# Optimization experiments

Hardware: AMD Instinct MI355X
Metric: run time of the kernel (lower is better)

The kernel has to match this reference:

```python
import jax, jax.numpy as jnp
import numpy as np

N_NODES = 100000


def gcn_conv(x, src, dst, W, b, n_nodes):
    # PyG GCNConv: linear transform, add self-loops, symmetric normalization,
    # scatter-add aggregation, then bias.
    h = x @ W  # [N, out]
    # append self-loops
    loop = jnp.arange(n_nodes, dtype=src.dtype)
    s = jnp.concatenate([src, loop])
    d = jnp.concatenate([dst, loop])
    # degree of destination nodes (edge weight 1)
    deg = jax.ops.segment_sum(jnp.ones_like(d, dtype=h.dtype), d, num_segments=n_nodes)
    dinv = jnp.where(deg > 0, jax.lax.rsqrt(deg), 0.0)
    norm = dinv[s] * dinv[d]  # [E+N]
    msg = norm[:, None] * h[s]  # gather + scale
    out = jax.ops.segment_sum(msg, d, num_segments=n_nodes)  # scatter-add
    return out + b


def setup_inputs() -> dict:
    key = jax.random.key(0)
    k1, k2, k3, k4, k5 = jax.random.split(key, 5)
    x = jax.random.normal(k1, (N_NODES, 128), dtype=jnp.float32)
    edge_index = jax.random.randint(k2, (2, 1600000), 0, N_NODES, dtype=jnp.int64)
    # Glorot-style init for GCN linear weights (bias zero, as in PyG default)
    W1 = jax.random.normal(k3, (128, 128), dtype=jnp.float32) * (1.0 / np.sqrt(128))
    b1 = jnp.zeros((128,), dtype=jnp.float32)
    W2 = jax.random.normal(k4, (128, 64), dtype=jnp.float32) * (1.0 / np.sqrt(128))
    b2 = jnp.zeros((64,), dtype=jnp.float32)
    return {"x": x, "edge_index": edge_index, "W1": W1, "b1": b1, "W2": W2, "b2": b2}


def reference(x, edge_index, W1, b1, W2, b2):
    src, dst = edge_index[0], edge_index[1]
    h = gcn_conv(x, src, dst, W1, b1, N_NODES)
    h = jax.nn.relu(h)
    # dropout p=0.5 with training=False -> identity (eval mode)
    out = gcn_conv(h, src, dst, W2, b2, N_NODES)
    return out
```

## Files before the change

### kernel.cpp

```cpp
#include <hip/hip_runtime.h>
#include <hip/hip_fp16.h>
#include <math.h>

#define NN 100000
#define BS 256
#define NB 391
#define NBLK 256
#define CAP 48
#define STAGE_CAP 5120

__global__ __launch_bounds__(256) void bucketA_k(const int* __restrict__ ei,
                                                 unsigned* __restrict__ edges,
                                                 unsigned* __restrict__ seg_cnt,
                                                 int E) {
    __shared__ unsigned cur[NB];
    const int tid = threadIdx.x;
    int odd = ei[2 * (tid & 63) + 1];
    const int st = (__ballot(odd != 0) == 0ull) ? 2 : 1;
    for (int i = tid; i < NB; i += 256) cur[i] = 0;
    __syncthreads();

    const int epb = (E + NBLK - 1) / NBLK;
    const int base = blockIdx.x * epb;
    const int end = min(base + epb, E);
    unsigned* __restrict__ reg = edges + (size_t)blockIdx.x * NB * CAP;

    if (st == 2) {
        const int2* __restrict__ e2 = (const int2*)ei;
        for (int i = base + tid; i < end; i += 256) {
            unsigned s = (unsigned)e2[i].x;
            unsigned d = (unsigned)e2[(size_t)E + i].x;
            unsigned bk = d >> 8;
            unsigned pos = atomicAdd(&cur[bk], 1u);
            if (pos < CAP) reg[bk * CAP + pos] = (s << 8) | (d & 255u);
        }
    } else {
        for (int i = base + tid; i < end; i += 256) {
            unsigned s = (unsigned)ei[i];
            unsigned d = (unsigned)ei[(size_t)E + i];
            unsigned bk = d >> 8;
            unsigned pos = atomicAdd(&cur[bk], 1u);
            if (pos < CAP) reg[bk * CAP + pos] = (s << 8) | (d & 255u);
        }
    }
    __syncthreads();
    for (int i = tid; i < NB; i += 256)
        seg_cnt[(size_t)blockIdx.x * NB + i] = min(cur[i], (unsigned)CAP);
}

__global__ __launch_bounds__(512) void bucketscan_k(const unsigned* __restrict__ seg_cnt,
                                                    unsigned* __restrict__ bucket_base,
                                                    unsigned* __restrict__ row_start) {
    __shared__ unsigned tot[512];
    const int k = threadIdx.x;
    unsigned s = 0;
    if (k < NB)
        for (int b = 0; b < NBLK; ++b) s += seg_cnt[(size_t)b * NB + k];
    tot[k] = s;
    __syncthreads();
    for (int off = 1; off < 512; off <<= 1) {
        unsigned v = tot[k];
        unsigned a = (k >= off) ? tot[k - off] : 0u;
        __syncthreads();
        tot[k] = v + a;
        __syncthreads();
    }
    if (k < NB) bucket_base[k] = tot[k] - s;
    if (k == 0) row_start[NN] = tot[NB - 1];
}

__global__ __launch_bounds__(256) void bucketB_k(const unsigned* __restrict__ edges,
                                                 const unsigned* __restrict__ seg_cnt,
                                                 const unsigned* __restrict__ bucket_base,
                                                 unsigned* __restrict__ csr_src,
                                                 unsigned* __restrict__ row_start,
                                                 float* __restrict__ dinv) {
    __shared__ unsigned stage[STAGE_CAP];
    __shared__ unsigned soff[NBLK];
    __shared__ unsigned scn[256];
    __shared__ unsigned cnt[BS];
    const int k = blockIdx.x, tid = threadIdx.x;

    unsigned sc = seg_cnt[(size_t)tid * NB + k];
    scn[tid] = sc;
    __syncthreads();
    for (int off = 1; off < 256; off <<= 1) {
        unsigned v = scn[tid];
        unsigned a = (tid >= off) ? scn[tid - off] : 0u;
        __syncthreads();
        scn[tid] = v + a;
        __syncthreads();
    }
    soff[tid] = scn[tid] - sc;
    __syncthreads();
    unsigned T = scn[255];
    if (T > STAGE_CAP) T = STAGE_CAP;

    for (unsigned j = tid; j < T; j += 256) {
        int lo = 0;
        #pragma unroll
        for (int stp = 128; stp > 0; stp >>= 1) {
            int m = lo + stp;
            if (m < NBLK && soff[m] <= j) lo = m;
        }
        unsigned elem = j - soff[lo];
        stage[j] = edges[((size_t)lo * NB + k) * CAP + elem];
    }
    for (int i = tid; i < BS; i += 256) cnt[i] = 0;
    __syncthreads();

    for (unsigned j = tid; j < T; j += 256) atomicAdd(&cnt[stage[j] & 255u], 1u);
    __syncthreads();

    unsigned c0 = cnt[tid];
    scn[tid] = c0;
    __syncthreads();
    for (int off = 1; off < 256; off <<= 1) {
        unsigned v = scn[tid];
        unsigned a = (tid >= off) ? scn[tid - off] : 0u;
        __syncthreads();
        scn[tid] = v + a;
        __syncthreads();
    }
    unsigned excl = scn[tid] - c0;
    const unsigned bbase = bucket_base[k];
    unsigned g0 = (unsigned)k * BS + tid;
    if (g0 < NN) {
        row_start[g0] = bbase + excl;
        dinv[g0] = rsqrtf((float)(c0 + 1u));
    }
    __syncthreads();
    cnt[tid] = excl;
    __syncthreads();

    for (unsigned j = tid; j < T; j += 256) {
        unsigned v = stage[j];
        unsigned pos = atomicAdd(&cnt[v & 255u], 1u);
        csr_src[bbase + pos] = v >> 8;
    }
}

template <int BN, int NT>
__global__ __launch_bounds__(NT) void gemm_k128(const float* __restrict__ X,
                                                const float* __restrict__ Wm,
                                                __half* __restrict__ H) {
    constexpr int TCN = BN / 4;
    constexpr int TRN = NT / TCN;
    constexpr int TM = 8;
    constexpr int BM = TRN * TM;
    constexpr int XP = BM + 4;
    __shared__ float ws[32 * BN];
    __shared__ float xsT[128 * XP];

    const int t = threadIdx.x;
    const int tc = t % TCN;
    const int tr = t / TCN;
    const int row0 = blockIdx.x * BM;

    for (int f = t; f < BM * 32; f += NT) {
        int r = f >> 5, c4 = f & 31;
        float4 v = make_float4(0.f, 0.f, 0.f, 0.f);
        if (row0 + r < NN) v = ((const float4*)(X + (size_t)(row0 + r) * 128))[c4];
        xsT[(c4 * 4 + 0) * XP + r] = v.x;
        xsT[(c4 * 4 + 1) * XP + r] = v.y;
        xsT[(c4 * 4 + 2) * XP + r] = v.z;
        xsT[(c4 * 4 + 3) * XP + r] = v.w;
    }

    float acc[TM][4] = {};
    for (int kc = 0; kc < 4; ++kc) {
        __syncthreads();
        for (int f = t; f < 32 * BN / 4; f += NT)
            ((float4*)ws)[f] = ((const float4*)Wm)[kc * (32 * BN / 4) + f];
        __syncthreads();
        #pragma unroll 4
        for (int k2 = 0; k2 < 32; ++k2) {
            float4 bv = *(const float4*)&ws[k2 * BN + tc * 4];
            const float* __restrict__ ar = &xsT[(kc * 32 + k2) * XP + tr * TM];
            #pragma unroll
            for (int m = 0; m < TM; ++m) {
                float a = ar[m];
                acc[m][0] = fmaf(a, bv.x, acc[m][0]);
                acc[m][1] = fmaf(a, bv.y, acc[m][1]);
                acc[m][2] = fmaf(a, bv.z, acc[m][2]);
                acc[m][3] = fmaf(a, bv.w, acc[m][3]);
            }
        }
    }
    #pragma unroll
    for (int m = 0; m < TM; ++m) {
        int r = row0 + tr * TM + m;
        if (r < NN) {
            __half2 p0 = __floats2half2_rn(acc[m][0], acc[m][1]);
            __half2 p1 = __floats2half2_rn(acc[m][2], acc[m][3]);
            uint2 w;
            w.x = *(unsigned*)&p0;
            w.y = *(unsigned*)&p1;
            ((uint2*)(H + (size_t)r * BN))[tc] = w;
        }
    }
}

template <int F, bool RELU>
__global__ __launch_bounds__(256) void aggregate_k(
    const __half* __restrict__ H, const unsigned* __restrict__ row_start,
    const unsigned* __restrict__ csr_src, const float* __restrict__ dinv,
    const float* __restrict__ bias, float* __restrict__ out) {
    const int wid = (blockIdx.x * blockDim.x + threadIdx.x) >> 6;
    const int lane = threadIdx.x & 63;
    if (wid >= NN) return;

    const float di = dinv[wid];
    const unsigned s0 = row_start[wid];
    const unsigned s1 = row_start[wid + 1];

    if constexpr (F == 128) {
        const __half2* __restrict__ H2 = (const __half2*)H;
        float2 h = __half22float2(H2[(size_t)wid * 64 + lane]);
        const float w0 = di * di;
        float2 acc = make_float2(w0 * h.x, w0 * h.y);
        unsigned e = s0;
        for (; e + 4 <= s1; e += 4) {
            unsigned i0 = csr_src[e], i1 = csr_src[e + 1];
            unsigned i2 = csr_src[e + 2], i3 = csr_src[e + 3];
            float2 h0 = __half22float2(H2[(size_t)i0 * 64 + lane]);
            float2 h1v = __half22float2(H2[(size_t)i1 * 64 + lane]);
            float2 h2v = __half22float2(H2[(size_t)i2 * 64 + lane]);
            float2 h3 = __half22float2(H2[(size_t)i3 * 64 + lane]);
            float wa = di * dinv[i0], wb = di * dinv[i1];
            float wc = di * dinv[i2], wd = di * dinv[i3];
            acc.x = fmaf(wa, h0.x, acc.x);  acc.y = fmaf(wa, h0.y, acc.y);
            acc.x = fmaf(wb, h1v.x, acc.x); acc.y = fmaf(wb, h1v.y, acc.y);
            acc.x = fmaf(wc, h2v.x, acc.x); acc.y = fmaf(wc, h2v.y, acc.y);
            acc.x = fmaf(wd, h3.x, acc.x);  acc.y = fmaf(wd, h3.y, acc.y);
        }
        for (; e < s1; ++e) {
            unsigned sa = csr_src[e];
            float wa = di * dinv[sa];
            float2 ha = __half22float2(H2[(size_t)sa * 64 + lane]);
            acc.x = fmaf(wa, ha.x, acc.x);
            acc.y = fmaf(wa, ha.y, acc.y);
        }
        float2 bv = ((const float2*)bias)[lane];
        acc.x += bv.x;
        acc.y += bv.y;
        if (RELU) {
            acc.x = fmaxf(acc.x, 0.0f);
            acc.y = fmaxf(acc.y, 0.0f);
        }
        ((float2*)out)[(size_t)wid * 64 + lane] = acc;
    } else {
        float h = __half2float(H[(size_t)wid * 64 + lane]);
        float acc = di * di * h;
        unsigned e = s0;
        for (; e + 4 <= s1; e += 4) {
            unsigned i0 = csr_src[e], i1 = csr_src[e + 1];
            unsigned i2 = csr_src[e + 2], i3 = csr_src[e + 3];
            float h0 = __half2float(H[(size_t)i0 * 64 + lane]);
            float h1v = __half2float(H[(size_t)i1 * 64 + lane]);
            float h2v = __half2float(H[(size_t)i2 * 64 + lane]);
            float h3 = __half2float(H[(size_t)i3 * 64 + lane]);
            acc = fmaf(di * dinv[i0], h0, acc);
            acc = fmaf(di * dinv[i1], h1v, acc);
            acc = fmaf(di * dinv[i2], h2v, acc);
            acc = fmaf(di * dinv[i3], h3, acc);
        }
        for (; e < s1; ++e) {
            unsigned sa = csr_src[e];
            acc = fmaf(di * dinv[sa], __half2float(H[(size_t)sa * 64 + lane]), acc);
        }
        acc += bias[lane];
        if (RELU) acc = fmaxf(acc, 0.0f);
        out[(size_t)wid * 64 + lane] = acc;
    }
}

extern "C" void kernel_launch(void* const* d_in, const int* in_sizes, int n_in,
                              void* d_out, int out_size, void* d_ws, size_t ws_size,
                              hipStream_t stream) {
    const float* x  = (const float*)d_in[0];
    const int*   ei = (const int*)d_in[1];
    const float* W1 = (const float*)d_in[2];
    const float* b1 = (const float*)d_in[3];
    const float* W2 = (const float*)d_in[4];
    const float* b2 = (const float*)d_in[5];
    float* out = (float*)d_out;
    const int E = in_sizes[1] / 2;

    char* p = (char*)d_ws;
    auto take = [&](size_t n) {
        char* r = p;
        p += (n + 255) & ~(size_t)255;
        return r;
    };
    __half*   h1        = (__half*)take((size_t)NN * 128 * 2);
    float*    o1        = (float*)take((size_t)NN * 128 * 4);
    unsigned* csr_src   = (unsigned*)take((size_t)E * 4);
    unsigned* row_start = (unsigned*)take((size_t)(NN + 1) * 4);
    float*    dinvp     = (float*)take((size_t)NN * 4);
    unsigned* seg_cnt   = (unsigned*)take((size_t)NBLK * NB * 4);
    unsigned* bbase     = (unsigned*)take((size_t)NB * 4);
    unsigned* edges     = (unsigned*)h1;
    __half*   h2        = h1;

    bucketA_k<<<NBLK, 256, 0, stream>>>(ei, edges, seg_cnt, E);
    bucketscan_k<<<1, 512, 0, stream>>>(seg_cnt, bbase, row_start);
    bucketB_k<<<NB, 256, 0, stream>>>(edges, seg_cnt, bbase, csr_src, row_start, dinvp);

    const int GEMM_GRID = (NN + 63) / 64;

    gemm_k128<128, 256><<<GEMM_GRID, 256, 0, stream>>>(x, W1, h1);
    aggregate_k<128, true><<<25000, 256, 0, stream>>>(h1, row_start, csr_src, dinvp, b1, o1);

    gemm_k128<64, 128><<<GEMM_GRID, 128, 0, stream>>>(o1, W2, h2);
    aggregate_k<64, false><<<25000, 256, 0, stream>>>(h2, row_start, csr_src, dinvp, b2, out);
}
```

Measured before the change: 388.9 us.

## Use MFMA fp16 GEMMs, fp16 intermediate activations, and deeper gather unrolling

Replaces the scalar fp32 register-tiled GEMMs with MFMA 16x16x32 f16 kernels. The inputs and a pre-transposed fp16 weight copy are staged in XOR-swizzled shared memory. The first-layer aggregation now writes its output in fp16, which halves the traffic for the second GEMM's input. The aggregation loops are unrolled to 8 neighbors, with all index and feature loads issued before the FMAs to expose more memory-level parallelism. The cost is extra fp16 rounding of x and of the hidden activations, plus a small extra weight-prep kernel launch.

```diff
diff --git a/kernel.cpp b/kernel.cpp
--- a/kernel.cpp
+++ b/kernel.cpp
@@ -8,6 +8,9 @@
 #define NBLK 256
 #define CAP 48
 #define STAGE_CAP 5120
+
+typedef _Float16 half8 __attribute__((ext_vector_type(8)));
+typedef float f32x4 __attribute__((ext_vector_type(4)));
 
 __global__ __launch_bounds__(256) void bucketA_k(const int* __restrict__ ei,
                                                  unsigned* __restrict__ edges,
@@ -140,72 +143,98 @@
     }
 }
 
-template <int BN, int NT>
-__global__ __launch_bounds__(NT) void gemm_k128(const float* __restrict__ X,
-                                                const float* __restrict__ Wm,
-                                                __half* __restrict__ H) {
-    constexpr int TCN = BN / 4;
-    constexpr int TRN = NT / TCN;
-    constexpr int TM = 8;
-    constexpr int BM = TRN * TM;
-    constexpr int XP = BM + 4;
-    __shared__ float ws[32 * BN];
-    __shared__ float xsT[128 * XP];
-
+__global__ __launch_bounds__(256) void prep_w_k(const float* __restrict__ W1,
+                                                const float* __restrict__ W2,
+                                                _Float16* __restrict__ w1t,
+                                                _Float16* __restrict__ w2t) {
     const int t = threadIdx.x;
-    const int tc = t % TCN;
-    const int tr = t / TCN;
-    const int row0 = blockIdx.x * BM;
-
-    for (int f = t; f < BM * 32; f += NT) {
-        int r = f >> 5, c4 = f & 31;
-        float4 v = make_float4(0.f, 0.f, 0.f, 0.f);
-        if (row0 + r < NN) v = ((const float4*)(X + (size_t)(row0 + r) * 128))[c4];
-        xsT[(c4 * 4 + 0) * XP + r] = v.x;
-        xsT[(c4 * 4 + 1) * XP + r] = v.y;
-        xsT[(c4 * 4 + 2) * XP + r] = v.z;
-        xsT[(c4 * 4 + 3) * XP + r] = v.w;
-    }
-
-    float acc[TM][4] = {};
+    if (blockIdx.x == 0) {
+        for (int i = t; i < 128 * 128; i += 256) {
+            int k = i >> 7, n = i & 127;
+            w1t[n * 128 + k] = (_Float16)W1[i];
+        }
+    } else {
+        for (int i = t; i < 128 * 64; i += 256) {
+            int k = i >> 6, n = i & 63;
+            w2t[n * 128 + k] = (_Float16)W2[i];
+        }
+    }
+}
+
+template <int BN, bool IN_F32>
+__global__ __launch_bounds__(256) void gemm_mfma_k(const void* __restrict__ Xv,
+                                                   const _Float16* __restrict__ Wt,
+                                                   _Float16* __restrict__ H) {
+    __shared__ _Float16 xs[64 * 128];
+    __shared__ _Float16 wsm[BN * 128];
+    char* xb = (char*)xs;
+    char* wb = (char*)wsm;
+    const int t = threadIdx.x;
+    const int row0 = blockIdx.x * 64;
+
+    if constexpr (IN_F32) {
+        const float* X = (const float*)Xv;
+        for (int f = t; f < 64 * 32; f += 256) {
+            int r = f >> 5, c4 = f & 31;
+            float4 v = make_float4(0.f, 0.f, 0.f, 0.f);
+            if (row0 + r < NN) v = ((const float4*)(X + (size_t)(row0 + r) * 128))[c4];
+            _Float16 h4[4] = {(_Float16)v.x, (_Float16)v.y, (_Float16)v.z, (_Float16)v.w};
+            int byte = (r * 256 + c4 * 8) ^ ((r & 7) << 4);
+            *(uint2*)(xb + byte) = *(uint2*)h4;
+        }
+    } else {
+        const _Float16* X = (const _Float16*)Xv;
+        for (int f = t; f < 64 * 16; f += 256) {
+            int r = f >> 4, c8 = f & 15;
+            uint4 v = make_uint4(0u, 0u, 0u, 0u);
+            if (row0 + r < NN) v = ((const uint4*)(X + (size_t)(row0 + r) * 128))[c8];
+            int byte = (r * 256 + c8 * 16) ^ ((r & 7) << 4);
+            *(uint4*)(xb + byte) = v;
+        }
+    }
+    for (int f = t; f < BN * 16; f += 256) {
+        int n = f >> 4, c8 = f & 15;
+        uint4 v = ((const uint4*)(Wt + (size_t)n * 128))[c8];
+        int byte = (n * 256 + c8 * 16) ^ ((n & 7) << 4);
+        *(uint4*)(wb + byte) = v;
+    }
+    __syncthreads();
+
+    const int w = t >> 6, l = t & 63;
+    const int lr = l & 15, lk = l >> 4;
+
+    f32x4 acc[BN / 16];
+    #pragma unroll
+    for (int n = 0; n < BN / 16; ++n) acc[n] = (f32x4){0.f, 0.f, 0.f, 0.f};
+
+    #pragma unroll
     for (int kc = 0; kc < 4; ++kc) {
-        __syncthreads();
-        for (int f = t; f < 32 * BN / 4; f += NT)
-            ((float4*)ws)[f] = ((const float4*)Wm)[kc * (32 * BN / 4) + f];
-        __syncthreads();
-        #pragma unroll 4
-        for (int k2 = 0; k2 < 32; ++k2) {
-            float4 bv = *(const float4*)&ws[k2 * BN + tc * 4];
-            const float* __restrict__ ar = &xsT[(kc * 32 + k2) * XP + tr * TM];
-            #pragma unroll
-            for (int m = 0; m < TM; ++m) {
-                float a = ar[m];
-                acc[m][0] = fmaf(a, bv.x, acc[m][0]);
-                acc[m][1] = fmaf(a, bv.y, acc[m][1]);
-                acc[m][2] = fmaf(a, bv.z, acc[m][2]);
-                acc[m][3] = fmaf(a, bv.w, acc[m][3]);
-            }
-        }
-    }
+        const int kbyte = kc * 64 + lk * 16;
+        const int ar = w * 16 + lr;
+        half8 a = *(const half8*)(xb + ((ar * 256 + kbyte) ^ ((ar & 7) << 4)));
+        #pragma unroll
+        for (int n = 0; n < BN / 16; ++n) {
+            const int bc = n * 16 + lr;
+            half8 b = *(const half8*)(wb + ((bc * 256 + kbyte) ^ ((bc & 7) << 4)));
+            acc[n] = __builtin_amdgcn_mfma_f32_16x16x32_f16(a, b, acc[n], 0, 0, 0);
+        }
+    }
+
     #pragma unroll
-    for (int m = 0; m < TM; ++m) {
-        int r = row0 + tr * TM + m;
-        if (r < NN) {
-            __half2 p0 = __floats2half2_rn(acc[m][0], acc[m][1]);
-            __half2 p1 = __floats2half2_rn(acc[m][2], acc[m][3]);
-            uint2 w;
-            w.x = *(unsigned*)&p0;
-            w.y = *(unsigned*)&p1;
-            ((uint2*)(H + (size_t)r * BN))[tc] = w;
-        }
-    }
-}
-
-template <int F, bool RELU>
+    for (int n = 0; n < BN / 16; ++n) {
+        #pragma unroll
+        for (int r = 0; r < 4; ++r) {
+            int rr = row0 + w * 16 + lk * 4 + r;
+            if (rr < NN) H[(size_t)rr * BN + n * 16 + lr] = (_Float16)acc[n][r];
+        }
+    }
+}
+
+template <int F, bool RELU, bool OUT_HALF>
 __global__ __launch_bounds__(256) void aggregate_k(
-    const __half* __restrict__ H, const unsigned* __restrict__ row_start,
+    const _Float16* __restrict__ H, const unsigned* __restrict__ row_start,
     const unsigned* __restrict__ csr_src, const float* __restrict__ dinv,
-    const float* __restrict__ bias, float* __restrict__ out) {
+    const float* __restrict__ bias, void* __restrict__ outv) {
     const int wid = (blockIdx.x * blockDim.x + threadIdx.x) >> 6;
     const int lane = threadIdx.x & 63;
     if (wid >= NN) return;
@@ -215,29 +244,35 @@
     const unsigned s1 = row_start[wid + 1];
 
     if constexpr (F == 128) {
-        const __half2* __restrict__ H2 = (const __half2*)H;
-        float2 h = __half22float2(H2[(size_t)wid * 64 + lane]);
+        const unsigned* __restrict__ H2 = (const unsigned*)H;
+        auto up = [](unsigned u) {
+            __half2 h = *(__half2*)&u;
+            return __half22float2(h);
+        };
+        float2 h = up(H2[(size_t)wid * 64 + lane]);
         const float w0 = di * di;
         float2 acc = make_float2(w0 * h.x, w0 * h.y);
         unsigned e = s0;
-        for (; e + 4 <= s1; e += 4) {
-            unsigned i0 = csr_src[e], i1 = csr_src[e + 1];
-            unsigned i2 = csr_src[e + 2], i3 = csr_src[e + 3];
-            float2 h0 = __half22float2(H2[(size_t)i0 * 64 + lane]);
-            float2 h1v = __half22float2(H2[(size_t)i1 * 64 + lane]);
-            float2 h2v = __half22float2(H2[(size_t)i2 * 64 + lane]);
-            float2 h3 = __half22float2(H2[(size_t)i3 * 64 + lane]);
-            float wa = di * dinv[i0], wb = di * dinv[i1];
-            float wc = di * dinv[i2], wd = di * dinv[i3];
-            acc.x = fmaf(wa, h0.x, acc.x);  acc.y = fmaf(wa, h0.y, acc.y);
-            acc.x = fmaf(wb, h1v.x, acc.x); acc.y = fmaf(wb, h1v.y, acc.y);
-            acc.x = fmaf(wc, h2v.x, acc.x); acc.y = fmaf(wc, h2v.y, acc.y);
-            acc.x = fmaf(wd, h3.x, acc.x);  acc.y = fmaf(wd, h3.y, acc.y);
+        for (; e + 8 <= s1; e += 8) {
+            unsigned idx[8], hv[8];
+            float wq[8];
+            #pragma unroll
+            for (int q = 0; q < 8; ++q) idx[q] = csr_src[e + q];
+            #pragma unroll
+            for (int q = 0; q < 8; ++q) hv[q] = H2[(size_t)idx[q] * 64 + lane];
+            #pragma unroll
+            for (int q = 0; q < 8; ++q) wq[q] = di * dinv[idx[q]];
+            #pragma unroll
+            for (int q = 0; q < 8; ++q) {
+                float2 hh = up(hv[q]);
+                acc.x = fmaf(wq[q], hh.x, acc.x);
+                acc.y = fmaf(wq[q], hh.y, acc.y);
+            }
         }
         for (; e < s1; ++e) {
             unsigned sa = csr_src[e];
             float wa = di * dinv[sa];
-            float2 ha = __half22float2(H2[(size_t)sa * 64 + lane]);
+            float2 ha = up(H2[(size_t)sa * 64 + lane]);
             acc.x = fmaf(wa, ha.x, acc.x);
             acc.y = fmaf(wa, ha.y, acc.y);
         }
@@ -248,30 +283,38 @@
             acc.x = fmaxf(acc.x, 0.0f);
             acc.y = fmaxf(acc.y, 0.0f);
         }
-        ((float2*)out)[(size_t)wid * 64 + lane] = acc;
+        if constexpr (OUT_HALF) {
+            __half2 o = __floats2half2_rn(acc.x, acc.y);
+            ((unsigned*)outv)[(size_t)wid * 64 + lane] = *(unsigned*)&o;
+        } else {
+            ((float2*)outv)[(size_t)wid * 64 + lane] = acc;
+        }
     } else {
-        float h = __half2float(H[(size_t)wid * 64 + lane]);
+        const unsigned short* __restrict__ Hs = (const unsigned short*)H;
+        auto up1 = [](unsigned short u) { return (float)*(_Float16*)&u; };
+        float h = up1(Hs[(size_t)wid * 64 + lane]);
         float acc = di * di * h;
         unsigned e = s0;
-        for (; e + 4 <= s1; e += 4) {
-            unsigned i0 = csr_src[e], i1 = csr_src[e + 1];
-            unsigned i2 = csr_src[e + 2], i3 = csr_src[e + 3];
-            float h0 = __half2float(H[(size_t)i0 * 64 + lane]);
-            float h1v = __half2float(H[(size_t)i1 * 64 + lane]);
-            float h2v = __half2float(H[(size_t)i2 * 64 + lane]);
-            float h3 = __half2float(H[(size_t)i3 * 64 + lane]);
-            acc = fmaf(di * dinv[i0], h0, acc);
-            acc = fmaf(di * dinv[i1], h1v, acc);
-            acc = fmaf(di * dinv[i2], h2v, acc);
-            acc = fmaf(di * dinv[i3], h3, acc);
+        for (; e + 8 <= s1; e += 8) {
+            unsigned idx[8];
+            unsigned short hv[8];
+            float wq[8];
+            #pragma unroll
+            for (int q = 0; q < 8; ++q) idx[q] = csr_src[e + q];
+            #pragma unroll
+            for (int q = 0; q < 8; ++q) hv[q] = Hs[(size_t)idx[q] * 64 + lane];
+            #pragma unroll
+            for (int q = 0; q < 8; ++q) wq[q] = di * dinv[idx[q]];
+            #pragma unroll
+            for (int q = 0; q < 8; ++q) acc = fmaf(wq[q], up1(hv[q]), acc);
         }
         for (; e < s1; ++e) {
             unsigned sa = csr_src[e];
-            acc = fmaf(di * dinv[sa], __half2float(H[(size_t)sa * 64 + lane]), acc);
+            acc = fmaf(di * dinv[sa], up1(Hs[(size_t)sa * 64 + lane]), acc);
         }
         acc += bias[lane];
         if (RELU) acc = fmaxf(acc, 0.0f);
-        out[(size_t)wid * 64 + lane] = acc;
+        ((float*)outv)[(size_t)wid * 64 + lane] = acc;
     }
 }
 
@@ -293,25 +336,28 @@
         p += (n + 255) & ~(size_t)255;
         return r;
     };
-    __half*   h1        = (__half*)take((size_t)NN * 128 * 2);
-    float*    o1        = (float*)take((size_t)NN * 128 * 4);
+    _Float16* h1        = (_Float16*)take((size_t)NN * 128 * 2);
+    _Float16* o1        = (_Float16*)take((size_t)NN * 128 * 2);
     unsigned* csr_src   = (unsigned*)take((size_t)E * 4);
     unsigned* row_start = (unsigned*)take((size_t)(NN + 1) * 4);
     float*    dinvp     = (float*)take((size_t)NN * 4);
     unsigned* seg_cnt   = (unsigned*)take((size_t)NBLK * NB * 4);
     unsigned* bbase     = (unsigned*)take((size_t)NB * 4);
+    _Float16* w1t       = (_Float16*)take((size_t)128 * 128 * 2);
+    _Float16* w2t       = (_Float16*)take((size_t)64 * 128 * 2);
     unsigned* edges     = (unsigned*)h1;
-    __half*   h2        = h1;
+    _Float16* h2        = h1;
 
     bucketA_k<<<NBLK, 256, 0, stream>>>(ei, edges, seg_cnt, E);
     bucketscan_k<<<1, 512, 0, stream>>>(seg_cnt, bbase, row_start);
     bucketB_k<<<NB, 256, 0, stream>>>(edges, seg_cnt, bbase, csr_src, row_start, dinvp);
-
-    const int GEMM_GRID = (NN + 63) / 64;
-
-    gemm_k128<128, 256><<<GEMM_GRID, 256, 0, stream>>>(x, W1, h1);
-    aggregate_k<128, true><<<25000, 256, 0, stream>>>(h1, row_start, csr_src, dinvp, b1, o1);
-
-    gemm_k128<64, 128><<<GEMM_GRID, 128, 0, stream>>>(o1, W2, h2);
-    aggregate_k<64, false><<<25000, 256, 0, stream>>>(h2, row_start, csr_src, dinvp, b2, out);
-}
+    prep_w_k<<<2, 256, 0, stream>>>(W1, W2, w1t, w2t);
+
+    const int GG = (NN + 63) / 64;
+
+    gemm_mfma_k<128, true><<<GG, 256, 0, stream>>>(x, w1t, h1);
+    aggregate_k<128, true, true><<<25000, 256, 0, stream>>>(h1, row_start, csr_src, dinvp, b1, o1);
+
+    gemm_mfma_k<64, false><<<GG, 256, 0, stream>>>(o1, w2t, h2);
+    aggregate_k<64, false, false><<<25000, 256, 0, stream>>>(h2, row_start, csr_src, dinvp, b2, out);
+}
```

After: 339.3 us. -12.7%, faster.
